# Kernel tuning notes

Hardware: AMD Instinct MI355X
Metric: run time of the kernel (lower is better)

## Reference

```python
import jax, jax.numpy as jnp
import numpy as np

N_NODES = 100000
N_EDGES = 1600000
D = 64
N_LAYERS = 3  # in -> h1 -> h2 -> out
LN_EPS = 1e-5


def setup_inputs() -> dict:
    key = jax.random.key(0)
    ks = jax.random.split(key, 4)
    scale = 1.0 / np.sqrt(D)
    vert_features = jax.random.normal(ks[0], (N_NODES, D), dtype=jnp.float32)
    edges = jax.random.randint(ks[1], (N_EDGES, 2), 0, N_NODES, dtype=jnp.int64)
    W0 = jax.random.normal(ks[2], (N_LAYERS, D, D), dtype=jnp.float32) * scale
    W1 = jax.random.normal(ks[3], (N_LAYERS, D, D), dtype=jnp.float32) * scale
    b0 = jnp.zeros((N_LAYERS, D), dtype=jnp.float32)
    b1 = jnp.zeros((N_LAYERS, D), dtype=jnp.float32)
    ln_gamma = jnp.ones((N_LAYERS - 1, D), dtype=jnp.float32)
    ln_beta = jnp.zeros((N_LAYERS - 1, D), dtype=jnp.float32)
    return {"vert_features": vert_features, "edges": edges, "W0": W0, "b0": b0,
            "W1": W1, "b1": b1, "ln_gamma": ln_gamma, "ln_beta": ln_beta}


def _graph_conv(h, src, dst, deg, W0l, b0l, W1l, b1l):
    # messages from every vertex, then undirected neighbor-mean aggregation
    msg = h @ W1l + b1l                                   # [N, D]
    idx = jnp.concatenate([dst, src])                     # both directions
    val = jnp.concatenate([msg[src], msg[dst]])           # [2E, D] gather
    agg = jax.ops.segment_sum(val, idx, num_segments=N_NODES)
    agg = agg / deg[:, None]                              # normalize=True
    return h @ W0l + b0l + agg


def _layer_norm(x, gamma, beta):
    mu = jnp.mean(x, axis=-1, keepdims=True)
    var = jnp.mean(jnp.square(x - mu), axis=-1, keepdims=True)
    return (x - mu) * jax.lax.rsqrt(var + LN_EPS) * gamma + beta


def reference(vert_features, edges, W0, b0, W1, b1, ln_gamma, ln_beta):
    src = edges[:, 0]
    dst = edges[:, 1]
    idx = jnp.concatenate([dst, src])
    deg = jax.ops.segment_sum(jnp.ones((2 * N_EDGES,), jnp.float32), idx,
                              num_segments=N_NODES)
    deg = jnp.maximum(deg, 1.0)
    h = vert_features
    for l in range(N_LAYERS - 1):
        h = _graph_conv(h, src, dst, deg, W0[l], b0[l], W1[l], b1[l])
        h = _layer_norm(h, ln_gamma[l], ln_beta[l])
        h = jax.nn.relu(h)
    h = _graph_conv(h, src, dst, deg, W0[-1], b0[-1], W1[-1], b1[-1])
    return h
```

## Files before the change

### kernel.cpp

```cpp
#include <hip/hip_runtime.h>
#include <hip/hip_bf16.h>

constexpr int D_ = 64;
constexpr int NN = 100000;
constexpr int NE = 1600000;
constexpr int RB = 8;

constexpr int BUCK_SH = 7;
constexpr int NBUCK = (NN + 127) >> BUCK_SH;
constexpr int NB1 = 256;
constexpr int NQ4 = NE / 4;
constexpr int QPB = (NQ4 + NB1 - 1) / NB1;
constexpr int SCN = NBUCK * NB1;
constexpr int SCB = (SCN + 1023) / 1024;

__device__ __forceinline__ float bflo(unsigned v) { return __uint_as_float(v << 16); }
__device__ __forceinline__ float bfhi(unsigned v) { return __uint_as_float(v & 0xffff0000u); }

__global__ __launch_bounds__(256) void k_s1count(const int* __restrict__ edges,
                                                 int* __restrict__ cnts) {
  __shared__ int hist[NBUCK];
  for (int i = threadIdx.x; i < NBUCK; i += 256) hist[i] = 0;
  __syncthreads();
  const int q0 = blockIdx.x * QPB;
  const int q1 = min(q0 + QPB, NQ4);
  for (int q = q0 + (int)threadIdx.x; q < q1; q += 256) {
    const int4* ep = reinterpret_cast<const int4*>(edges + 8 * q);
    int4 a = ep[0], b = ep[1];
    atomicAdd(&hist[a.x >> BUCK_SH], 1);
    atomicAdd(&hist[a.y >> BUCK_SH], 1);
    atomicAdd(&hist[a.z >> BUCK_SH], 1);
    atomicAdd(&hist[a.w >> BUCK_SH], 1);
    atomicAdd(&hist[b.x >> BUCK_SH], 1);
    atomicAdd(&hist[b.y >> BUCK_SH], 1);
    atomicAdd(&hist[b.z >> BUCK_SH], 1);
    atomicAdd(&hist[b.w >> BUCK_SH], 1);
  }
  __syncthreads();
  for (int i = threadIdx.x; i < NBUCK; i += 256)
    cnts[i * NB1 + blockIdx.x] = hist[i];
}

__global__ __launch_bounds__(1024) void k_scanA(const int* __restrict__ cnt,
                                                int* __restrict__ oscan,
                                                int* __restrict__ bsum, int n) {
  __shared__ int sd[1024];
  const int tid = threadIdx.x;
  const int i = blockIdx.x * 1024 + tid;
  int v = (i < n) ? cnt[i] : 0;
  sd[tid] = v;
  __syncthreads();
  for (int off = 1; off < 1024; off <<= 1) {
    int t = (tid >= off) ? sd[tid - off] : 0;
    __syncthreads();
    sd[tid] += t;
    __syncthreads();
  }
  if (i < n) oscan[i] = sd[tid] - v;
  if (tid == 1023) bsum[blockIdx.x] = sd[1023];
}

__global__ __launch_bounds__(256) void k_scanB(int* __restrict__ bsum, int nb) {
  __shared__ int sd[256];
  const int tid = threadIdx.x;
  int v = (tid < nb) ? bsum[tid] : 0;
  sd[tid] = v;
  __syncthreads();
  for (int off = 1; off < 256; off <<= 1) {
    int t = (tid >= off) ? sd[tid - off] : 0;
    __syncthreads();
    sd[tid] += t;
    __syncthreads();
  }
  if (tid < nb) bsum[tid] = sd[tid] - v;
}

__global__ __launch_bounds__(256) void k_scanC(int* __restrict__ oscan,
                                               const int* __restrict__ bsum, int n) {
  int i = blockIdx.x * 256 + threadIdx.x;
  if (i < n) oscan[i] += bsum[i >> 10];
}

__global__ __launch_bounds__(256) void k_s1scatter(const int* __restrict__ edges,
                                                   const int* __restrict__ sscan,
                                                   unsigned* __restrict__ items) {
  __shared__ int cur[NBUCK];
  for (int i = threadIdx.x; i < NBUCK; i += 256)
    cur[i] = sscan[i * NB1 + blockIdx.x];
  __syncthreads();
  const int q0 = blockIdx.x * QPB;
  const int q1 = min(q0 + QPB, NQ4);
  for (int q = q0 + (int)threadIdx.x; q < q1; q += 256) {
    const int4* ep = reinterpret_cast<const int4*>(edges + 8 * q);
    int4 a = ep[0], b = ep[1];
    int p;
    p = atomicAdd(&cur[a.y >> BUCK_SH], 1); items[p] = ((unsigned)(a.y & 127) << 17) | (unsigned)a.x;
    p = atomicAdd(&cur[a.x >> BUCK_SH], 1); items[p] = ((unsigned)(a.x & 127) << 17) | (unsigned)a.y;
    p = atomicAdd(&cur[a.w >> BUCK_SH], 1); items[p] = ((unsigned)(a.w & 127) << 17) | (unsigned)a.z;
    p = atomicAdd(&cur[a.z >> BUCK_SH], 1); items[p] = ((unsigned)(a.z & 127) << 17) | (unsigned)a.w;
    p = atomicAdd(&cur[b.y >> BUCK_SH], 1); items[p] = ((unsigned)(b.y & 127) << 17) | (unsigned)b.x;
    p = atomicAdd(&cur[b.x >> BUCK_SH], 1); items[p] = ((unsigned)(b.x & 127) << 17) | (unsigned)b.y;
    p = atomicAdd(&cur[b.w >> BUCK_SH], 1); items[p] = ((unsigned)(b.w & 127) << 17) | (unsigned)b.z;
    p = atomicAdd(&cur[b.z >> BUCK_SH], 1); items[p] = ((unsigned)(b.z & 127) << 17) | (unsigned)b.w;
  }
}

__global__ __launch_bounds__(256) void k_s2build(const unsigned* __restrict__ items,
                                                 const int* __restrict__ sscan,
                                                 int* __restrict__ offs,
                                                 int* __restrict__ nbr) {
  const int b = blockIdx.x;
  const int lo = b << BUCK_SH;
  __shared__ int hist[128], scn[128];
  __shared__ int sbase, send;
  if (threadIdx.x == 0) {
    sbase = sscan[b * NB1];
    send = (b + 1 < NBUCK) ? sscan[(b + 1) * NB1] : 2 * NE;
  }
  if (threadIdx.x < 128) hist[threadIdx.x] = 0;
  __syncthreads();
  const int i0 = sbase, i1 = send;
  for (int i = i0 + (int)threadIdx.x; i < i1; i += 256)
    atomicAdd(&hist[items[i] >> 17], 1);
  __syncthreads();
  if (threadIdx.x < 128) scn[threadIdx.x] = hist[threadIdx.x];
  __syncthreads();
  for (int off = 1; off < 128; off <<= 1) {
    int t = (threadIdx.x < 128 && (int)threadIdx.x >= off) ? scn[threadIdx.x - off] : 0;
    __syncthreads();
    if (threadIdx.x < 128) scn[threadIdx.x] += t;
    __syncthreads();
  }
  if (threadIdx.x < 128) {
    int node = lo + threadIdx.x;
    int ex = sbase + scn[threadIdx.x] - hist[threadIdx.x];
    if (node < NN) offs[node] = ex;
    hist[threadIdx.x] = ex;
  }
  __syncthreads();
  for (int i = i0 + (int)threadIdx.x; i < i1; i += 256) {
    unsigned it = items[i];
    int pos = atomicAdd(&hist[it >> 17], 1);
    nbr[pos] = (int)(it & 0x1FFFFu);
  }
  if (b == 0 && threadIdx.x == 0) offs[NN] = 2 * NE;
}

__device__ __forceinline__ void stage_w(const float* __restrict__ W, float* wT) {
  for (int i = threadIdx.x; i < 4096; i += 256) {
    int k = i >> 6, j = i & 63;
    wT[j * 68 + k] = W[i];
  }
}

__global__ __launch_bounds__(256) void k_gemm2(
    const float* __restrict__ h, const float* __restrict__ W0,
    const float* __restrict__ b0, const float* __restrict__ W1,
    const float* __restrict__ b1, float* __restrict__ base,
    __hip_bfloat16* __restrict__ msg, int nrows) {
  __shared__ float w0T[64 * 68];
  __shared__ float w1T[64 * 68];
  __shared__ float rbuf[4][RB * 64];
  stage_w(W0, w0T);
  stage_w(W1, w1T);
  __syncthreads();
  const int lane = threadIdx.x & 63;
  const int wv = threadIdx.x >> 6;
  const int wid = (blockIdx.x * 256 + threadIdx.x) >> 6;
  const int nw = (gridDim.x * 256) >> 6;
  const float bv0 = b0[lane], bv1 = b1[lane];
  const float4* wl0 = reinterpret_cast<const float4*>(&w0T[lane * 68]);
  const float4* wl1 = reinterpret_cast<const float4*>(&w1T[lane * 68]);
  float* myrows = rbuf[wv];

  const int chunk = (nrows + nw - 1) / nw;
  const int r0 = wid * chunk;
  const int r1 = min(r0 + chunk, nrows);
  if (r0 >= nrows) return;

  float st[RB];
#pragma unroll
  for (int rr = 0; rr < RB; ++rr) {
    int r = min(r0 + rr, nrows - 1);
    st[rr] = h[(size_t)r * 64 + lane];
  }
  for (int rb = r0; rb < r1; rb += RB) {
#pragma unroll
    for (int rr = 0; rr < RB; ++rr) myrows[rr * 64 + lane] = st[rr];
    const int nb = rb + RB;
    if (nb < r1) {
#pragma unroll
      for (int rr = 0; rr < RB; ++rr) {
        int r = min(nb + rr, nrows - 1);
        st[rr] = h[(size_t)r * 64 + lane];
      }
    }
    float a0[RB], a1[RB];
#pragma unroll
    for (int rr = 0; rr < RB; ++rr) { a0[rr] = bv0; a1[rr] = bv1; }
#pragma unroll 1
    for (int k4 = 0; k4 < 16; ++k4) {
      const float4 v0 = wl0[k4];
      const float4 v1 = wl1[k4];
#pragma unroll
      for (int rr = 0; rr < RB; ++rr) {
        float4 hv = *reinterpret_cast<const float4*>(&myrows[rr * 64 + k4 * 4]);
        a0[rr] = fmaf(hv.x, v0.x, a0[rr]); a1[rr] = fmaf(hv.x, v1.x, a1[rr]);
        a0[rr] = fmaf(hv.y, v0.y, a0[rr]); a1[rr] = fmaf(hv.y, v1.y, a1[rr]);
        a0[rr] = fmaf(hv.z, v0.z, a0[rr]); a1[rr] = fmaf(hv.z, v1.z, a1[rr]);
        a0[rr] = fmaf(hv.w, v0.w, a0[rr]); a1[rr] = fmaf(hv.w, v1.w, a1[rr]);
      }
    }
#pragma unroll
    for (int rr = 0; rr < RB; ++rr) {
      int r = rb + rr;
      if (r < r1) {
        base[(size_t)r * 64 + lane] = a0[rr];
        msg[(size_t)r * 64 + lane] = __float2bfloat16(a1[rr]);
      }
    }
  }
}

template <bool LN>
__global__ __launch_bounds__(256) void k_agg(
    const float* __restrict__ base, const __hip_bfloat16* __restrict__ msg,
    const int* __restrict__ offs, const int* __restrict__ nbr,
    const float* __restrict__ gamma, const float* __restrict__ beta,
    float* __restrict__ out, int nrows) {
  const int lane = threadIdx.x & 63;
  const int half = lane >> 5;
  const int c = lane & 31;
  const int wid = (blockIdx.x * 256 + threadIdx.x) >> 6;
  const int nw = (gridDim.x * 256) >> 6;
  float gm = 1.0f, bt = 0.0f;
  if (LN) { gm = gamma[lane]; bt = beta[lane]; }
  const unsigned* msg32 = reinterpret_cast<const unsigned*>(msg);
  for (int r = wid; r < nrows; r += nw) {
    const int n0 = offs[r], n1 = offs[r + 1];
    const float bval = base[(size_t)r * 64 + lane];
    float agx = 0.0f, agy = 0.0f;
    for (int jb = n0; jb < n1; jb += 32) {
      int idx[16];
#pragma unroll
      for (int u = 0; u < 16; ++u) {
        int jj = jb + 2 * u + half;
        idx[u] = nbr[min(jj, n1 - 1)];
      }
      unsigned mv[16];
#pragma unroll
      for (int u = 0; u < 16; ++u) mv[u] = msg32[(idx[u] << 5) + c];
#pragma unroll
      for (int u = 0; u < 16; ++u) {
        if (jb + 2 * u + half >= n1) mv[u] = 0u;
        agx += bflo(mv[u]);
        agy += bfhi(mv[u]);
      }
    }
    agx += __shfl_xor(agx, 32, 64);
    agy += __shfl_xor(agy, 32, 64);
    float tx = __shfl(agx, lane >> 1, 64);
    float ty = __shfl(agy, lane >> 1, 64);
    float ag = (lane & 1) ? ty : tx;
    const float rdeg = 1.0f / fmaxf((float)(n1 - n0), 1.0f);
    float val = fmaf(ag, rdeg, bval);
    if (LN) {
      float s = val;
#pragma unroll
      for (int off = 32; off > 0; off >>= 1) s += __shfl_xor(s, off, 64);
      const float mu = s * (1.0f / 64.0f);
      const float dv = val - mu;
      float v2 = dv * dv;
#pragma unroll
      for (int off = 32; off > 0; off >>= 1) v2 += __shfl_xor(v2, off, 64);
      const float var = v2 * (1.0f / 64.0f);
      val = fmaxf(fmaf(dv * rsqrtf(var + 1e-5f), gm, bt), 0.0f);
    }
    out[(size_t)r * 64 + lane] = val;
  }
}

extern "C" void kernel_launch(void* const* d_in, const int* in_sizes, int n_in,
                              void* d_out, int out_size, void* d_ws, size_t ws_size,
                              hipStream_t stream) {
  const float* vert = (const float*)d_in[0];
  const int* edges = (const int*)d_in[1];
  const float* W0 = (const float*)d_in[2];
  const float* b0 = (const float*)d_in[3];
  const float* W1 = (const float*)d_in[4];
  const float* b1 = (const float*)d_in[5];
  const float* lng = (const float*)d_in[6];
  const float* lnb = (const float*)d_in[7];
  float* base = (float*)d_out;

  const size_t HB = (size_t)NN * D_ * sizeof(float);
  float* hbuf = (float*)d_ws;
  int* nbr = (int*)((char*)d_ws + HB);
  char* msgreg = (char*)d_ws + HB + (size_t)2 * NE * 4;
  __hip_bfloat16* msg = (__hip_bfloat16*)msgreg;
  unsigned* items = (unsigned*)msgreg;
  int* offs = (int*)((char*)d_ws + HB + (size_t)2 * NE * 4 + HB / 2);
  int* cnts = (int*)d_out;
  int* sscan = cnts + SCN;
  int* bsum = sscan + SCN;

  k_s1count<<<NB1, 256, 0, stream>>>(edges, cnts);
  k_scanA<<<SCB, 1024, 0, stream>>>(cnts, sscan, bsum, SCN);
  k_scanB<<<1, 256, 0, stream>>>(bsum, SCB);
  k_scanC<<<(SCN + 255) / 256, 256, 0, stream>>>(sscan, bsum, SCN);
  k_s1scatter<<<NB1, 256, 0, stream>>>(edges, sscan, items);
  k_s2build<<<NBUCK, 256, 0, stream>>>(items, sscan, offs, nbr);

  const int GB = 2048;
  const int GG = 1024;

  for (int l = 0; l < 3; ++l) {
    const float* hcur = (l == 0) ? vert : hbuf;
    k_gemm2<<<GG, 256, 0, stream>>>(hcur, W0 + l * 4096, b0 + l * 64,
                                    W1 + l * 4096, b1 + l * 64, base, msg, NN);
    if (l < 2) {
      k_agg<true><<<GB, 256, 0, stream>>>(base, msg, offs, nbr,
                                          lng + l * 64, lnb + l * 64, hbuf, NN);
    } else {
      k_agg<false><<<GB, 256, 0, stream>>>(base, msg, offs, nbr,
                                           nullptr, nullptr, base, NN);
    }
  }
}
```

Baseline: 420.4 us.

## Fuse aggregation+LayerNorm with next layer's dual GEMM, ping-pong message buffers

```diff
diff --git a/kernel.cpp b/kernel.cpp
--- a/kernel.cpp
+++ b/kernel.cpp
@@ -153,6 +153,43 @@
   }
 }
 
+__device__ __forceinline__ float gather_row(const unsigned* __restrict__ msg32,
+                                            const int* __restrict__ nbr,
+                                            int n0, int n1, int half, int c,
+                                            int lane) {
+  float agx = 0.0f, agy = 0.0f;
+  int jb = n0;
+  for (; jb + 32 <= n1; jb += 32) {
+    int idx[16];
+#pragma unroll
+    for (int u = 0; u < 16; ++u) idx[u] = nbr[jb + 2 * u + half];
+    unsigned mv[16];
+#pragma unroll
+    for (int u = 0; u < 16; ++u) mv[u] = msg32[(idx[u] << 5) + c];
+#pragma unroll
+    for (int u = 0; u < 16; ++u) { agx += bflo(mv[u]); agy += bfhi(mv[u]); }
+  }
+  if (jb < n1) {
+    int idx[16];
+#pragma unroll
+    for (int u = 0; u < 16; ++u) idx[u] = nbr[min(jb + 2 * u + half, n1 - 1)];
+    unsigned mv[16];
+#pragma unroll
+    for (int u = 0; u < 16; ++u) mv[u] = msg32[(idx[u] << 5) + c];
+#pragma unroll
+    for (int u = 0; u < 16; ++u) {
+      if (jb + 2 * u + half >= n1) mv[u] = 0u;
+      agx += bflo(mv[u]);
+      agy += bfhi(mv[u]);
+    }
+  }
+  agx += __shfl_xor(agx, 32, 64);
+  agy += __shfl_xor(agy, 32, 64);
+  float tx = __shfl(agx, lane >> 1, 64);
+  float ty = __shfl(agy, lane >> 1, 64);
+  return (lane & 1) ? ty : tx;
+}
+
 __global__ __launch_bounds__(256) void k_gemm2(
     const float* __restrict__ h, const float* __restrict__ W0,
     const float* __restrict__ b0, const float* __restrict__ W1,
@@ -222,61 +259,101 @@
   }
 }
 
-template <bool LN>
-__global__ __launch_bounds__(256) void k_agg(
-    const float* __restrict__ base, const __hip_bfloat16* __restrict__ msg,
+__global__ __launch_bounds__(256) void k_fused(
+    float* __restrict__ base, const __hip_bfloat16* __restrict__ msgin,
+    __hip_bfloat16* __restrict__ msgout,
     const int* __restrict__ offs, const int* __restrict__ nbr,
     const float* __restrict__ gamma, const float* __restrict__ beta,
-    float* __restrict__ out, int nrows) {
+    const float* __restrict__ W0n, const float* __restrict__ b0n,
+    const float* __restrict__ W1n, const float* __restrict__ b1n, int nrows) {
+  __shared__ float w0T[64 * 68];
+  __shared__ float w1T[64 * 68];
+  __shared__ float rbuf[4][RB * 64];
+  stage_w(W0n, w0T);
+  stage_w(W1n, w1T);
+  __syncthreads();
+  const int lane = threadIdx.x & 63;
+  const int wv = threadIdx.x >> 6;
+  const int half = lane >> 5;
+  const int c = lane & 31;
+  const int wid = (blockIdx.x * 256 + threadIdx.x) >> 6;
+  const int nw = (gridDim.x * 256) >> 6;
+  const float gm = gamma[lane], bt = beta[lane];
+  const float bv0 = b0n[lane], bv1 = b1n[lane];
+  const float4* wl0 = reinterpret_cast<const float4*>(&w0T[lane * 68]);
+  const float4* wl1 = reinterpret_cast<const float4*>(&w1T[lane * 68]);
+  float* myrows = rbuf[wv];
+  const unsigned* msg32 = reinterpret_cast<const unsigned*>(msgin);
+
+  const int chunk = (nrows + nw - 1) / nw;
+  const int r0 = wid * chunk;
+  const int r1 = min(r0 + chunk, nrows);
+  if (r0 >= nrows) return;
+
+  for (int rb = r0; rb < r1; rb += RB) {
+#pragma unroll 1
+    for (int rr = 0; rr < RB; ++rr) {
+      int r = rb + rr;
+      if (r >= r1) break;
+      const int n0 = offs[r], n1 = offs[r + 1];
+      const float bval = base[(size_t)r * 64 + lane];
+      float ag = gather_row(msg32, nbr, n0, n1, half, c, lane);
+      const float rdeg = 1.0f / fmaxf((float)(n1 - n0), 1.0f);
+      float val = fmaf(ag, rdeg, bval);
+      float s = val;
+#pragma unroll
+      for (int off = 32; off > 0; off >>= 1) s += __shfl_xor(s, off, 64);
+      const float mu = s * (1.0f / 64.0f);
+      const float dv = val - mu;
+      float v2 = dv * dv;
+#pragma unroll
+      for (int off = 32; off > 0; off >>= 1) v2 += __shfl_xor(v2, off, 64);
+      const float var = v2 * (1.0f / 64.0f);
+      val = fmaxf(fmaf(dv * rsqrtf(var + 1e-5f), gm, bt), 0.0f);
+      myrows[rr * 64 + lane] = val;
+    }
+    float a0[RB], a1[RB];
+#pragma unroll
+    for (int rr = 0; rr < RB; ++rr) { a0[rr] = bv0; a1[rr] = bv1; }
+#pragma unroll 1
+    for (int k4 = 0; k4 < 16; ++k4) {
+      const float4 v0 = wl0[k4];
+      const float4 v1 = wl1[k4];
+#pragma unroll
+      for (int rr = 0; rr < RB; ++rr) {
+        float4 hv = *reinterpret_cast<const float4*>(&myrows[rr * 64 + k4 * 4]);
+        a0[rr] = fmaf(hv.x, v0.x, a0[rr]); a1[rr] = fmaf(hv.x, v1.x, a1[rr]);
+        a0[rr] = fmaf(hv.y, v0.y, a0[rr]); a1[rr] = fmaf(hv.y, v1.y, a1[rr]);
+        a0[rr] = fmaf(hv.z, v0.z, a0[rr]); a1[rr] = fmaf(hv.z, v1.z, a1[rr]);
+        a0[rr] = fmaf(hv.w, v0.w, a0[rr]); a1[rr] = fmaf(hv.w, v1.w, a1[rr]);
+      }
+    }
+#pragma unroll
+    for (int rr = 0; rr < RB; ++rr) {
+      int r = rb + rr;
+      if (r < r1) {
+        base[(size_t)r * 64 + lane] = a0[rr];
+        msgout[(size_t)r * 64 + lane] = __float2bfloat16(a1[rr]);
+      }
+    }
+  }
+}
+
+__global__ __launch_bounds__(256) void k_aggF(
+    float* __restrict__ base, const __hip_bfloat16* __restrict__ msg,
+    const int* __restrict__ offs, const int* __restrict__ nbr, int nrows) {
   const int lane = threadIdx.x & 63;
   const int half = lane >> 5;
   const int c = lane & 31;
   const int wid = (blockIdx.x * 256 + threadIdx.x) >> 6;
   const int nw = (gridDim.x * 256) >> 6;
-  float gm = 1.0f, bt = 0.0f;
-  if (LN) { gm = gamma[lane]; bt = beta[lane]; }
   const unsigned* msg32 = reinterpret_cast<const unsigned*>(msg);
   for (int r = wid; r < nrows; r += nw) {
     const int n0 = offs[r], n1 = offs[r + 1];
     const float bval = base[(size_t)r * 64 + lane];
-    float agx = 0.0f, agy = 0.0f;
-    for (int jb = n0; jb < n1; jb += 32) {
-      int idx[16];
-#pragma unroll
-      for (int u = 0; u < 16; ++u) {
-        int jj = jb + 2 * u + half;
-        idx[u] = nbr[min(jj, n1 - 1)];
-      }
-      unsigned mv[16];
-#pragma unroll
-      for (int u = 0; u < 16; ++u) mv[u] = msg32[(idx[u] << 5) + c];
-#pragma unroll
-      for (int u = 0; u < 16; ++u) {
-        if (jb + 2 * u + half >= n1) mv[u] = 0u;
-        agx += bflo(mv[u]);
-        agy += bfhi(mv[u]);
-      }
-    }
-    agx += __shfl_xor(agx, 32, 64);
-    agy += __shfl_xor(agy, 32, 64);
-    float tx = __shfl(agx, lane >> 1, 64);
-    float ty = __shfl(agy, lane >> 1, 64);
-    float ag = (lane & 1) ? ty : tx;
+    float ag = gather_row(msg32, nbr, n0, n1, half, c, lane);
     const float rdeg = 1.0f / fmaxf((float)(n1 - n0), 1.0f);
-    float val = fmaf(ag, rdeg, bval);
-    if (LN) {
-      float s = val;
-#pragma unroll
-      for (int off = 32; off > 0; off >>= 1) s += __shfl_xor(s, off, 64);
-      const float mu = s * (1.0f / 64.0f);
-      const float dv = val - mu;
-      float v2 = dv * dv;
-#pragma unroll
-      for (int off = 32; off > 0; off >>= 1) v2 += __shfl_xor(v2, off, 64);
-      const float var = v2 * (1.0f / 64.0f);
-      val = fmaxf(fmaf(dv * rsqrtf(var + 1e-5f), gm, bt), 0.0f);
-    }
-    out[(size_t)r * 64 + lane] = val;
+    base[(size_t)r * 64 + lane] = fmaf(ag, rdeg, bval);
   }
 }
 
@@ -293,13 +370,15 @@
   const float* lnb = (const float*)d_in[7];
   float* base = (float*)d_out;
 
-  const size_t HB = (size_t)NN * D_ * sizeof(float);
-  float* hbuf = (float*)d_ws;
-  int* nbr = (int*)((char*)d_ws + HB);
-  char* msgreg = (char*)d_ws + HB + (size_t)2 * NE * 4;
-  __hip_bfloat16* msg = (__hip_bfloat16*)msgreg;
-  unsigned* items = (unsigned*)msgreg;
-  int* offs = (int*)((char*)d_ws + HB + (size_t)2 * NE * 4 + HB / 2);
+  const size_t NBR_B = (size_t)2 * NE * 4;
+  const size_t MSG_B = (size_t)NN * 64 * 2;
+  int* nbr = (int*)d_ws;
+  char* msgAreg = (char*)d_ws + NBR_B;
+  char* msgBreg = msgAreg + MSG_B;
+  __hip_bfloat16* msgA = (__hip_bfloat16*)msgAreg;
+  __hip_bfloat16* msgB = (__hip_bfloat16*)msgBreg;
+  unsigned* items = (unsigned*)msgAreg;
+  int* offs = (int*)(msgBreg + MSG_B);
   int* cnts = (int*)d_out;
   int* sscan = cnts + SCN;
   int* bsum = sscan + SCN;
@@ -311,19 +390,16 @@
   k_s1scatter<<<NB1, 256, 0, stream>>>(edges, sscan, items);
   k_s2build<<<NBUCK, 256, 0, stream>>>(items, sscan, offs, nbr);
 
-  const int GB = 2048;
   const int GG = 1024;
-
-  for (int l = 0; l < 3; ++l) {
-    const float* hcur = (l == 0) ? vert : hbuf;
-    k_gemm2<<<GG, 256, 0, stream>>>(hcur, W0 + l * 4096, b0 + l * 64,
-                                    W1 + l * 4096, b1 + l * 64, base, msg, NN);
-    if (l < 2) {
-      k_agg<true><<<GB, 256, 0, stream>>>(base, msg, offs, nbr,
-                                          lng + l * 64, lnb + l * 64, hbuf, NN);
-    } else {
-      k_agg<false><<<GB, 256, 0, stream>>>(base, msg, offs, nbr,
-                                           nullptr, nullptr, base, NN);
-    }
-  }
-}
+  const int GF = 768;
+  const int GA = 2048;
+
+  k_gemm2<<<GG, 256, 0, stream>>>(vert, W0, b0, W1, b1, base, msgA, NN);
+  k_fused<<<GF, 256, 0, stream>>>(base, msgA, msgB, offs, nbr,
+                                  lng, lnb, W0 + 4096, b0 + 64,
+                                  W1 + 4096, b1 + 64, NN);
+  k_fused<<<GF, 256, 0, stream>>>(base, msgB, msgA, offs, nbr,
+                                  lng + 64, lnb + 64, W0 + 8192, b0 + 128,
+                                  W1 + 8192, b1 + 128, NN);
+  k_aggF<<<GA, 256, 0, stream>>>(base, msgA, offs, nbr, NN);
+}
```

Result: faster. 398.0 us (-5.3%).
